# Optimization experiments

Hardware: AMD Instinct MI355X
Metric: run time of the kernel (lower is better)

The kernel has to match this reference:

```python
import jax, jax.numpy as jnp
import numpy as np

# dims derived from init_kwargs
N_NODES = 100000            # type_mask.shape[0]
N0, N1 = 60000, 40000       # nodes per type
F0, F1 = 128, 64            # feats_dim_list
HID = 64                    # hidden_dim (= in_dim of layer1)
HEADS = 8
OUT = 16
ATTN_VEC = 128
E = 250000                  # metapath instances per metapath
L = 3                       # nodes per metapath instance (2 edge types)
NG = 8192                   # nodes in each minibatch DGL graph
B = 8192                    # number of target nodes
ETYPES = [[0, 1], [2, 3]]   # etypes_list; num_edge_type=4, RotatE0 -> 2 base relations


def setup_inputs() -> dict:
    ks = jax.random.split(jax.random.key(0), 20)
    g = lambda k, s, sc=1.0: sc * jax.random.normal(k, s, dtype=jnp.float32)
    return {
        "feat0": g(ks[0], (N0, F0)),
        "feat1": g(ks[1], (N1, F1)),
        "W0": g(ks[2], (HID, F0), 0.12),
        "b0": jnp.zeros((HID,), jnp.float32),
        "W1": g(ks[3], (HID, F1), 0.15),
        "b1": jnp.zeros((HID,), jnp.float32),
        "r_vec": g(ks[4], (2, HID // 2, 2), 0.2),
        "attn0": g(ks[5], (HEADS, HID), 0.2),
        "attn1": g(ks[6], (HEADS, HID), 0.2),
        "fc1_w": g(ks[7], (ATTN_VEC, HEADS * HID), 0.06),
        "fc1_b": jnp.zeros((ATTN_VEC,), jnp.float32),
        "fc2_w": g(ks[8], (1, ATTN_VEC), 0.1),
        "fc_w": g(ks[9], (OUT, HEADS * HID), 0.06),
        "fc_b": jnp.zeros((OUT,), jnp.float32),
        "idx0": jnp.arange(N0, dtype=jnp.int32),                 # type-0 node ids (contiguous block)
        "idx1": jnp.arange(N1, dtype=jnp.int32) + N0,            # type-1 node ids (offset block)
        "mp0_indices": jax.random.randint(ks[10], (E, L), 0, N_NODES, dtype=jnp.int32),
        "mp0_dst": jax.random.randint(ks[11], (E,), 0, NG, dtype=jnp.int32),
        "mp0_target": jax.random.randint(ks[12], (B,), 0, NG, dtype=jnp.int32),
        "mp1_indices": jax.random.randint(ks[13], (E, L), 0, N_NODES, dtype=jnp.int32),
        "mp1_dst": jax.random.randint(ks[14], (E,), 0, NG, dtype=jnp.int32),
        "mp1_target": jax.random.randint(ks[15], (B,), 0, NG, dtype=jnp.int32),
    }


def _cmul(a, b):
    # complex multiply on trailing dim of size 2
    re = a[..., 0] * b[..., 0] - a[..., 1] * b[..., 1]
    im = a[..., 0] * b[..., 1] + a[..., 1] * b[..., 0]
    return jnp.stack([re, im], axis=-1)


def reference(feat0, feat1, W0, b0, W1, b1, r_vec, attn0, attn1,
              fc1_w, fc1_b, fc2_w, fc_w, fc_b,
              idx0, idx1,
              mp0_indices, mp0_dst, mp0_target,
              mp1_indices, mp1_dst, mp1_target):
    # per-node-type linear scattered into a dense [N, HID] table (dropout=0 / eval)
    tf = jnp.zeros((N_NODES, HID), jnp.float32)
    tf = tf.at[idx0].set(feat0 @ W0.T + b0)
    tf = tf.at[idx1].set(feat1 @ W1.T + b1)

    # RotatE0: unit-modulus normalize, then double relations with conjugates
    rv = r_vec / jnp.linalg.norm(r_vec, axis=-1, keepdims=True)          # [2, HID//2, 2]
    conj = rv * jnp.array([1.0, -1.0], rv.dtype)
    rv_full = jnp.stack([rv, conj], axis=1).reshape(-1, HID // 2, 2)     # [4, HID//2, 2]

    def metapath(indices, dst, target, attn, etypes):
        edata = tf[indices].reshape(E, L, HID // 2, 2)   # gather metapath instances
        # suffix products of rotations: final[i] = prod_{j>=i} r[etypes[j]], final[L-1]=1
        final = [jnp.stack([jnp.ones(HID // 2, jnp.float32),
                            jnp.zeros(HID // 2, jnp.float32)], -1)]
        for i in range(L - 2, -1, -1):
            final.insert(0, _cmul(final[0], rv_full[etypes[i]]))
        finals = jnp.stack(final, axis=0)                # [L, HID//2, 2]
        edata = _cmul(edata, finals)                     # rotate every path position
        h = edata.reshape(E, L, HID).mean(axis=1)        # [E, HID] instance encoding
        # node-level attention (heads share h: torch tiles hidden across heads)
        a = jax.nn.leaky_relu(h @ attn.T, 0.01)          # [E, HEADS]
        m = jax.ops.segment_max(a, dst, num_segments=NG)
        ex = jnp.exp(a - m[dst])
        s = jax.ops.segment_sum(ex, dst, num_segments=NG)
        an = ex / s[dst]                                 # edge softmax per destination
        eft = jnp.einsum('eh,ed->ehd', an, h)            # [E, HEADS, HID]
        ft = jax.ops.segment_sum(eft, dst, num_segments=NG)
        ret = ft[target].reshape(B, HEADS * HID)
        return jax.nn.elu(ret)

    out0 = metapath(mp0_indices, mp0_dst, mp0_target, attn0, ETYPES[0])
    out1 = metapath(mp1_indices, mp1_dst, mp1_target, attn1, ETYPES[1])

    # metapath-level attention
    outs = jnp.stack([out0, out1], axis=0)               # [P, B, HEADS*HID]
    s1 = jnp.tanh(outs @ fc1_w.T + fc1_b)                # [P, B, ATTN_VEC]
    beta = jax.nn.softmax((s1.mean(axis=1) @ fc2_w.T)[:, 0], axis=0)  # [P]
    hagg = jnp.einsum('p,pbf->bf', beta, outs)           # [B, HEADS*HID]
    logits = hagg @ fc_w.T + fc_b                        # [B, OUT]
    return logits, hagg
```

## Files before the change

kernel.cpp:

```cpp
#include <hip/hip_runtime.h>
#include <hip/hip_fp16.h>
#include <math.h>

#define NNODES 100000
#define NT0 60000
#define NT1 40000
#define FD0 128
#define FD1 64
#define HID 64
#define HEADS 8
#define OUTD 16
#define AVEC 128
#define NE 250000
#define NG 8192
#define NB 8192

typedef _Float16 half8v __attribute__((ext_vector_type(8)));
typedef float f32x4 __attribute__((ext_vector_type(4)));

#define OFF_TF16    0ull
#define OFF_FINALS  3200000ull
#define OFF_ACC     3200512ull
#define OFF_BETA    3200768ull
#define OFF_WC0     3201024ull
#define OFF_WC1     3208192ull
#define OFF_BC0     3211776ull
#define OFF_BC1     3211904ull
#define OFF_FC1H    3212032ull
#define OFF_P       3244800ull
#define OFF_SORTED  5644800ull
#define OFF_COUNTS  7644800ull
#define OFF_CNTT    7661184ull
#define OFF_CURS    7677568ull
#define OFF_OFFS    7693952ull
#define OFF_FT16    7710592ull

__device__ __forceinline__ float2 rot_pair(const float* r_vec, int pi, int j){
  const float2* rv = (const float2*)r_vec;
  int rel = pi >= 3 ? 1 : 0;
  float2 r = rv[rel*32 + j];
  float n = rsqrtf(r.x*r.x + r.y*r.y);
  r.x *= n; r.y *= n;
  float2 rf = make_float2(r.x, -r.y);
  int pos = pi - rel*3;
  if (pos == 2) return make_float2(1.f, 0.f);
  if (pos == 1) return rf;
  return make_float2(rf.x*r.x - rf.y*r.y, rf.x*r.y + rf.y*r.x);
}

__global__ __launch_bounds__(128) void k_wcat(const float* __restrict__ r_vec,
     const float* __restrict__ attn0, const float* __restrict__ attn1,
     const float* __restrict__ W0v, const float* __restrict__ b0v,
     const float* __restrict__ W1v, const float* __restrict__ b1v,
     const float* __restrict__ fc1_w,
     __half* __restrict__ wc0, float* __restrict__ bc0,
     __half* __restrict__ wc1, float* __restrict__ bc1,
     __half* __restrict__ fc1h,
     float* __restrict__ finals, float* __restrict__ acc, float* __restrict__ beta){
  int bid = blockIdx.x;
  int t = threadIdx.x;
  if (bid == 288){
    if (t < 32){
      float2* F = (float2*)finals;
      #pragma unroll
      for (int pi = 0; pi < 6; ++pi) F[pi*32 + t] = rot_pair(r_vec, pi, t);
    }
    for (int q = t; q < 256; q += 128) acc[q] = 0.f;
    if (t < 2) beta[t] = 0.f;
    return;
  }
  if (bid >= 224){
    int base = (bid - 224)*1024;
    for (int i = t; i < 1024; i += 128)
      fc1h[base + i] = __float2half(fc1_w[base + i]);
    return;
  }
  int type = bid >= 112;
  int c = bid - type*112;
  int F = type ? FD1 : FD0;
  const float* W  = type ? W1v : W0v;
  const float* bv = type ? b1v : b0v;
  __half* wc = type ? wc1 : wc0;
  float* bc  = type ? bc1 : bc0;

  if (c < 64){
    for (int f = t; f < F; f += 128) wc[(size_t)c*F + f] = __float2half(W[(size_t)c*F + f]);
    if (t == 0) bc[c] = bv[c];
    return;
  }
  __shared__ float a[64];
  int cg = c - 64;
  int pi = cg >> 3, k = cg & 7;
  if (t < 32){
    float2 f = rot_pair(r_vec, pi, t);
    const float* at = (pi >= 3) ? attn1 : attn0;
    float a0 = at[k*64 + 2*t], a1 = at[k*64 + 2*t + 1];
    a[2*t]     = (f.x*a0 + f.y*a1) * (1.f/3.f);
    a[2*t + 1] = (f.x*a1 - f.y*a0) * (1.f/3.f);
  }
  __syncthreads();
  for (int f = t; f < F; f += 128){
    float s = 0.f;
    #pragma unroll 16
    for (int d = 0; d < 64; ++d) s += a[d] * W[(size_t)d*F + f];
    wc[(size_t)c*F + f] = __float2half(s);
  }
  if (t == 0){
    float s = 0.f;
    #pragma unroll 16
    for (int d = 0; d < 64; ++d) s += a[d] * bv[d];
    bc[c] = s;
  }
}

__global__ __launch_bounds__(256) void k_tform(const float* __restrict__ feat0,
      const int* __restrict__ idx0, const float* __restrict__ feat1,
      const int* __restrict__ idx1,
      const __half* __restrict__ wc0, const float* __restrict__ bc0,
      const __half* __restrict__ wc1, const float* __restrict__ bc1,
      __half* __restrict__ tf16, __half* __restrict__ P){
  const int nb0 = (NT0 + 63)/64;
  int bid = blockIdx.x;
  const float* feat; const int* idx; const __half* wc; const float* bc;
  int n_nodes, F, m0;
  if (bid < nb0){ feat=feat0; idx=idx0; wc=wc0; bc=bc0; n_nodes=NT0; F=FD0; m0=bid*64; }
  else { feat=feat1; idx=idx1; wc=wc1; bc=bc1; n_nodes=NT1; F=FD1; m0=(bid-nb0)*64; }
  __shared__ int idxs[64];
  __shared__ __half outs[64][120];
  int t = threadIdx.x;
  if (t < 64){
    int gm = m0 + t; if (gm > n_nodes - 1) gm = n_nodes - 1;
    idxs[t] = idx[gm];
  }
  __syncthreads();
  int w = t >> 6, l = t & 63;
  int lr = l & 15, lk = l >> 4;
  int gr = m0 + w*16 + lr; if (gr > n_nodes - 1) gr = n_nodes - 1;
  const float* arow = feat + (size_t)gr*F;

  f32x4 acc7[7];
  #pragma unroll
  for (int ct = 0; ct < 7; ++ct) acc7[ct] = (f32x4){0.f,0.f,0.f,0.f};

  int nk = F >> 5;
  for (int kk = 0; kk < nk; ++kk){
    int koff = kk*32 + lk*8;
    float4 ua = *(const float4*)(arow + koff);
    float4 ub = *(const float4*)(arow + koff + 4);
    half8v a = {(_Float16)ua.x,(_Float16)ua.y,(_Float16)ua.z,(_Float16)ua.w,
                (_Float16)ub.x,(_Float16)ub.y,(_Float16)ub.z,(_Float16)ub.w};
    #pragma unroll
    for (int ct = 0; ct < 7; ++ct){
      half8v b = *(const half8v*)(wc + (size_t)(ct*16 + lr)*F + koff);
      acc7[ct] = __builtin_amdgcn_mfma_f32_16x16x32_f16(a, b, acc7[ct], 0, 0, 0);
    }
  }

  #pragma unroll
  for (int ct = 0; ct < 7; ++ct){
    int col = ct*16 + lr;
    float bvv = bc[col];
    #pragma unroll
    for (int r = 0; r < 4; ++r){
      int nl = w*16 + lk*4 + r;
      outs[nl][col] = __float2half(acc7[ct][r] + bvv);
    }
  }
  __syncthreads();
  #pragma unroll
  for (int u = t; u < 512; u += 256){
    int n = u >> 3, c = u & 7;
    if (m0 + n < n_nodes){
      uint4 v = *(uint4*)&outs[n][c*8];
      *(uint4*)&tf16[(size_t)idxs[n]*64 + c*8] = v;
    }
  }
  for (int u = t; u < 384; u += 256){
    int pp = u >= 192;
    int rr = u - pp*192;
    int n = rr / 3, c = rr - n*3;
    if (m0 + n < n_nodes){
      uint4 v = *(uint4*)&outs[n][64 + pp*24 + c*8];
      *(uint4*)&P[(size_t)pp*2400000 + (size_t)idxs[n]*24 + c*8] = v;
    }
  }
}

__global__ void k_hist3(const int* __restrict__ d0, const int* __restrict__ d1,
                        const int* __restrict__ t0, const int* __restrict__ t1,
                        int* __restrict__ counts, int* __restrict__ cntt){
  int e = blockIdx.x*blockDim.x + threadIdx.x;
  if (e < NE) atomicAdd(&counts[d0[e]], 1);
  else if (e < 2*NE) atomicAdd(&counts[NG + d1[e-NE]], 1);
  else if (e < 2*NE + NB) atomicAdd(&cntt[t0[e-2*NE]], 1);
  else if (e < 2*NE + 2*NB) atomicAdd(&cntt[NG + t1[e-2*NE-NB]], 1);
}

__global__ __launch_bounds__(1024) void k_scan(const int* __restrict__ counts,
                                               int* __restrict__ offs,
                                               int* __restrict__ curs){
  __shared__ int lds[1024];
  int t = threadIdx.x;
  int base = t*16;
  int v[16]; int sum = 0;
  #pragma unroll
  for (int i = 0; i < 16; ++i){ v[i] = counts[base+i]; sum += v[i]; }
  lds[t] = sum;
  __syncthreads();
  for (int off = 1; off < 1024; off <<= 1){
    int x = (t >= off) ? lds[t-off] : 0;
    __syncthreads();
    lds[t] += x;
    __syncthreads();
  }
  int excl = lds[t] - sum;
  #pragma unroll
  for (int i = 0; i < 16; ++i){ offs[base+i] = excl; excl += v[i]; curs[base+i] = 0; }
  if (t == 1023) offs[2*NG] = excl;
}

__global__ void k_scatter2(const int* __restrict__ m0, const int* __restrict__ d0,
                           const int* __restrict__ m1, const int* __restrict__ d1,
                           const int* __restrict__ offs, int* __restrict__ curs,
                           int4* __restrict__ sorted){
  int e = blockIdx.x*blockDim.x + threadIdx.x;
  if (e >= 2*NE) return;
  const int* mp; int d;
  if (e < NE){ mp = m0 + (size_t)e*3; d = d0[e]; }
  else { mp = m1 + (size_t)(e-NE)*3; d = NG + d1[e-NE]; }
  int pos = offs[d] + atomicAdd(&curs[d], 1);
  sorted[pos] = make_int4(mp[0], mp[1], mp[2], 0);
}

__global__ __launch_bounds__(128) void k_seg(const __half* __restrict__ tf16,
                                             const __half* __restrict__ P,
                                             const int4* __restrict__ sorted,
                                             const int* __restrict__ offs,
                                             const float* __restrict__ finals,
                                             __half* __restrict__ ft16o){
  __shared__ int4 ndb[2][64];
  __shared__ float wb[2][64][8];
  int wv = threadIdx.x >> 6;
  int seg = blockIdx.x*2 + wv;
  int p = seg >> 13;
  int lane = threadIdx.x & 63;
  int hw = lane >> 5, j = lane & 31;
  int start = offs[seg], end = offs[seg+1];
  __half2* ftw = (__half2*)(ft16o + (size_t)seg*512);
  if (start == end){
    #pragma unroll
    for (int kk = 0; kk < 4; ++kk) ftw[(hw*4+kk)*32 + j] = __floats2half2_rn(0.f, 0.f);
    return;
  }
  const float2* F2 = (const float2*)(finals + p*192);
  float2 f0 = F2[j], f1 = F2[32 + j];
  const __half2* tfh = (const __half2*)tf16;
  const __half* Pp = P + (size_t)p*2400000;
  int4* nb = ndb[wv];
  float (*wbp)[8] = wb[wv];

  float sA[8], ur[8], ui[8];
  #pragma unroll
  for (int k = 0; k < 8; ++k){ sA[k] = 0.f; ur[k] = 0.f; ui[k] = 0.f; }

  for (int c = start; c < end; c += 64){
    int n = end - c; if (n > 64) n = 64;
    if (lane < n){
      int4 nd = sorted[c + lane];
      nb[lane] = nd;
      float4 rA = *(const float4*)(Pp + (size_t)nd.x*24);
      float4 rB = *(const float4*)(Pp + (size_t)nd.y*24 + 8);
      float4 rC = *(const float4*)(Pp + (size_t)nd.z*24 + 16);
      const __half2* ha = (const __half2*)&rA;
      const __half2* hb = (const __half2*)&rB;
      const __half2* hc = (const __half2*)&rC;
      float w[8];
      #pragma unroll
      for (int m = 0; m < 4; ++m){
        float2 va = __half22float2(ha[m]);
        float2 vb = __half22float2(hb[m]);
        float2 vc = __half22float2(hc[m]);
        float x0 = va.x + vb.x + vc.x;
        float x1 = va.y + vb.y + vc.y;
        x0 = x0 > 0.f ? x0 : 0.01f*x0;
        x1 = x1 > 0.f ? x1 : 0.01f*x1;
        w[2*m]   = __expf(x0);
        w[2*m+1] = __expf(x1);
      }
      #pragma unroll
      for (int k = 0; k < 8; ++k) sA[k] += w[k];
      *(float4*)&wbp[lane][0] = make_float4(w[0], w[1], w[2], w[3]);
      *(float4*)&wbp[lane][4] = make_float4(w[4], w[5], w[6], w[7]);
    }
    asm volatile("s_waitcnt lgkmcnt(0)" ::: "memory");
    __builtin_amdgcn_sched_barrier(0);
    int cend = c + n;
    for (int i = c + hw; i < cend; i += 2){
      int e = i - c;
      int4 nd = nb[e];
      float4 wlo = *(const float4*)&wbp[e][0];
      float4 whi = *(const float4*)&wbp[e][4];
      float2 v0 = __half22float2(tfh[(size_t)nd.x*32 + j]);
      float2 v1 = __half22float2(tfh[(size_t)nd.y*32 + j]);
      float2 v2 = __half22float2(tfh[(size_t)nd.z*32 + j]);
      float hre = (v0.x*f0.x - v0.y*f0.y) + (v1.x*f1.x - v1.y*f1.y) + v2.x;
      float him = (v0.x*f0.y + v0.y*f0.x) + (v1.x*f1.y + v1.y*f1.x) + v2.y;
      ur[0] += wlo.x*hre; ui[0] += wlo.x*him;
      ur[1] += wlo.y*hre; ui[1] += wlo.y*him;
      ur[2] += wlo.z*hre; ui[2] += wlo.z*him;
      ur[3] += wlo.w*hre; ui[3] += wlo.w*him;
      ur[4] += whi.x*hre; ui[4] += whi.x*him;
      ur[5] += whi.y*hre; ui[5] += whi.y*him;
      ur[6] += whi.z*hre; ui[6] += whi.z*him;
      ur[7] += whi.w*hre; ui[7] += whi.w*him;
    }
    asm volatile("s_waitcnt lgkmcnt(0)" ::: "memory");
    __builtin_amdgcn_sched_barrier(0);
  }
  #pragma unroll
  for (int k = 0; k < 8; ++k){
    ur[k] += __shfl_xor(ur[k], 32);
    ui[k] += __shfl_xor(ui[k], 32);
    float v = sA[k];
    #pragma unroll
    for (int mask = 1; mask < 64; mask <<= 1) v += __shfl_xor(v, mask);
    sA[k] = v;
  }
  #pragma unroll
  for (int kk = 0; kk < 4; ++kk){
    int k = hw*4 + kk;
    float inv = 1.f / (3.f * sA[k]);
    float re = ur[k]*inv, im = ui[k]*inv;
    re = re > 0.f ? re : expm1f(re);
    im = im > 0.f ? im : expm1f(im);
    ftw[k*32 + j] = __floats2half2_rn(re, im);
  }
}

__global__ __launch_bounds__(256) void k_s1g(const __half* __restrict__ ft16o,
                                             const int* __restrict__ cntt,
                                             const __half* __restrict__ fc1h,
                                             const float* __restrict__ fc1_b,
                                             float* __restrict__ acc_p){
  int bid = blockIdx.x;
  int p  = bid >> 8;
  int rb = bid & 255;
  int t = threadIdx.x;
  int w = t >> 6, l = t & 63;
  int rowbase = rb*32 + (w & 1)*16;
  int colbase = (w >> 1)*64;
  int lr = l & 15, lk = l >> 4;

  const half8v* Ab = (const half8v*)(ft16o + ((size_t)p*NG + rowbase)*512);
  f32x4 acc[4] = {{0.f,0.f,0.f,0.f},{0.f,0.f,0.f,0.f},
                  {0.f,0.f,0.f,0.f},{0.f,0.f,0.f,0.f}};

  #pragma unroll 4
  for (int kk = 0; kk < 16; ++kk){
    half8v a = Ab[(size_t)lr*64 + kk*4 + lk];
    #pragma unroll
    for (int ct = 0; ct < 4; ++ct){
      const half8v* Bb = (const half8v*)(fc1h + (size_t)(colbase + ct*16 + lr)*512);
      half8v b = Bb[kk*4 + lk];
      acc[ct] = __builtin_amdgcn_mfma_f32_16x16x32_f16(a, b, acc[ct], 0, 0, 0);
    }
  }

  float cf[4];
  #pragma unroll
  for (int r = 0; r < 4; ++r)
    cf[r] = (float)cntt[p*NG + rowbase + lk*4 + r];
  #pragma unroll
  for (int ct = 0; ct < 4; ++ct){
    int col = colbase + ct*16 + lr;
    float bv = fc1_b[col];
    float sv = 0.f;
    #pragma unroll
    for (int r = 0; r < 4; ++r)
      sv += cf[r] * tanhf(acc[ct][r] + bv);
    sv += __shfl_xor(sv, 16);
    sv += __shfl_xor(sv, 32);
    if (l < 16) atomicAdd(&acc_p[p*128 + col], sv);
  }
}

__global__ void k_beta(const float* __restrict__ acc, const float* __restrict__ fc2_w,
                       float* __restrict__ beta){
  int t = threadIdx.x;
  float s0 = acc[t]*fc2_w[t] + acc[t+64]*fc2_w[t+64];
  float s1 = acc[128+t]*fc2_w[t] + acc[192+t]*fc2_w[t+64];
  #pragma unroll
  for (int mask = 1; mask < 64; mask <<= 1){
    s0 += __shfl_xor(s0, mask, 64);
    s1 += __shfl_xor(s1, mask, 64);
  }
  if (t == 0){
    float z0 = s0 / (float)NB, z1 = s1 / (float)NB;
    float mz = fmaxf(z0, z1);
    float e0 = expf(z0 - mz), e1 = expf(z1 - mz);
    float inv = 1.f / (e0 + e1);
    beta[0] = e0*inv; beta[1] = e1*inv;
  }
}

__global__ void k_final(const __half* __restrict__ ft0, const __half* __restrict__ ft1,
                        const int* __restrict__ tgt0, const int* __restrict__ tgt1,
                        const float* __restrict__ beta, const float* __restrict__ fc_w,
                        const float* __restrict__ fc_b, float* __restrict__ d_out){
  __shared__ float lds[512];
  int b = blockIdx.x, t = threadIdx.x;
  float b0 = beta[0], b1 = beta[1];
  int g0 = tgt0[b], g1 = tgt1[b];
  float v0 = __half2float(ft0[(size_t)g0*512 + t]);
  float v1 = __half2float(ft1[(size_t)g1*512 + t]);
  float h = b0*v0 + b1*v1;
  lds[t] = h;
  d_out[(size_t)NB*OUTD + (size_t)b*512 + t] = h;
  __syncthreads();
  int o = t >> 5, j = t & 31;
  float s = 0.f;
  const float* w = fc_w + o*512;
  for (int d = j; d < 512; d += 32) s += lds[d]*w[d];
  #pragma unroll
  for (int mask = 1; mask < 32; mask <<= 1) s += __shfl_xor(s, mask, 32);
  if (j == 0) d_out[(size_t)b*OUTD + o] = s + fc_b[o];
}

extern "C" void kernel_launch(void* const* d_in, const int* in_sizes, int n_in,
                              void* d_out, int out_size, void* d_ws, size_t ws_size,
                              hipStream_t stream){
  const float* feat0  = (const float*)d_in[0];
  const float* feat1  = (const float*)d_in[1];
  const float* W0     = (const float*)d_in[2];
  const float* b0     = (const float*)d_in[3];
  const float* W1     = (const float*)d_in[4];
  const float* b1     = (const float*)d_in[5];
  const float* r_vec  = (const float*)d_in[6];
  const float* attn0  = (const float*)d_in[7];
  const float* attn1  = (const float*)d_in[8];
  const float* fc1_w  = (const float*)d_in[9];
  const float* fc1_b  = (const float*)d_in[10];
  const float* fc2_w  = (const float*)d_in[11];
  const float* fc_w   = (const float*)d_in[12];
  const float* fc_b   = (const float*)d_in[13];
  const int*   idx0   = (const int*)d_in[14];
  const int*   idx1   = (const int*)d_in[15];
  const int*   mpi0   = (const int*)d_in[16];
  const int*   mdst0  = (const int*)d_in[17];
  const int*   mtgt0  = (const int*)d_in[18];
  const int*   mpi1   = (const int*)d_in[19];
  const int*   mdst1  = (const int*)d_in[20];
  const int*   mtgt1  = (const int*)d_in[21];

  float* ws      = (float*)d_ws;
  __half* tf16   = (__half*)(ws + OFF_TF16);
  float* finals  = ws + OFF_FINALS;
  float* acc     = ws + OFF_ACC;
  float* beta    = ws + OFF_BETA;
  __half* wc0    = (__half*)(ws + OFF_WC0);
  __half* wc1    = (__half*)(ws + OFF_WC1);
  float* bc0     = ws + OFF_BC0;
  float* bc1     = ws + OFF_BC1;
  __half* fc1h   = (__half*)(ws + OFF_FC1H);
  __half* P      = (__half*)(ws + OFF_P);
  int4*  sorted  = (int4*)(ws + OFF_SORTED);
  int*   counts  = (int*)(ws + OFF_COUNTS);
  int*   cntt    = (int*)(ws + OFF_CNTT);
  int*   curs    = (int*)(ws + OFF_CURS);
  int*   offs    = (int*)(ws + OFF_OFFS);
  __half* ft16o  = (__half*)(ws + OFF_FT16);
  __half* ft0h   = ft16o;
  __half* ft1h   = ft16o + (size_t)NG*512;

  k_wcat<<<289, 128, 0, stream>>>(r_vec, attn0, attn1, W0, b0, W1, b1, fc1_w,
                                  wc0, bc0, wc1, bc1, fc1h, finals, acc, beta);
  hipMemsetAsync(counts, 0, 2*16384*sizeof(int), stream);
  k_hist3<<<(2*NE + 2*NB + 255)/256, 256, 0, stream>>>(mdst0, mdst1, mtgt0, mtgt1,
                                                       counts, cntt);
  k_scan<<<1, 1024, 0, stream>>>(counts, offs, curs);
  k_scatter2<<<(2*NE + 255)/256, 256, 0, stream>>>(mpi0, mdst0, mpi1, mdst1,
                                                   offs, curs, sorted);

  k_tform<<<(NT0 + 63)/64 + (NT1 + 63)/64, 256, 0, stream>>>(
      feat0, idx0, feat1, idx1, wc0, bc0, wc1, bc1, tf16, P);

  k_seg<<<NG, 128, 0, stream>>>(tf16, P, sorted, offs, finals, ft16o);

  k_s1g<<<512, 256, 0, stream>>>(ft16o, cntt, fc1h, fc1_b, acc);
  k_beta<<<1, 64, 0, stream>>>(acc, fc2_w, beta);
  k_final<<<NB, 512, 0, stream>>>(ft0h, ft1h, mtgt0, mtgt1, beta, fc_w, fc_b,
                                  (float*)d_out);
}
```

Before: 225.6 us.

## Precompute per-node output projection via MFMA and fold memset into setup kernel

The final fc projection is linear, so it is applied to every segment node's features inside the fc1 MFMA kernel, with an extra MFMA accumulator on half the waves. The final kernel then combines two 16-wide rows per target using beta instead of running a 512-wide dot product through LDS. The counts memset and the fc_w fp16 conversion move into extra blocks of the setup kernel, which removes an API call. An unroll pragma is also added to the segment aggregation loop. The trade-off is fp16 weights for the output projection and more work in k_s1g.

```diff
diff --git a/kernel.cpp b/kernel.cpp
--- a/kernel.cpp
+++ b/kernel.cpp
@@ -34,6 +34,8 @@
 #define OFF_CURS    7677568ull
 #define OFF_OFFS    7693952ull
 #define OFF_FT16    7710592ull
+#define OFF_L       11904896ull
+#define OFF_FCWH    12167040ull
 
 __device__ __forceinline__ float2 rot_pair(const float* r_vec, int pi, int j){
   const float2* rv = (const float2*)r_vec;
@@ -52,13 +54,24 @@
      const float* __restrict__ attn0, const float* __restrict__ attn1,
      const float* __restrict__ W0v, const float* __restrict__ b0v,
      const float* __restrict__ W1v, const float* __restrict__ b1v,
-     const float* __restrict__ fc1_w,
+     const float* __restrict__ fc1_w, const float* __restrict__ fc_w,
      __half* __restrict__ wc0, float* __restrict__ bc0,
      __half* __restrict__ wc1, float* __restrict__ bc1,
-     __half* __restrict__ fc1h,
+     __half* __restrict__ fc1h, __half* __restrict__ fcwh,
+     int* __restrict__ counts,
      float* __restrict__ finals, float* __restrict__ acc, float* __restrict__ beta){
   int bid = blockIdx.x;
   int t = threadIdx.x;
+  if (bid == 297){
+    for (int i = t; i < OUTD*512; i += 128) fcwh[i] = __float2half(fc_w[i]);
+    return;
+  }
+  if (bid >= 289){
+    int base = (bid - 289)*4096;
+    #pragma unroll
+    for (int i = t; i < 4096; i += 128) counts[base + i] = 0;
+    return;
+  }
   if (bid == 288){
     if (t < 32){
       float2* F = (float2*)finals;
@@ -295,6 +308,7 @@
     asm volatile("s_waitcnt lgkmcnt(0)" ::: "memory");
     __builtin_amdgcn_sched_barrier(0);
     int cend = c + n;
+    #pragma unroll 2
     for (int i = c + hw; i < cend; i += 2){
       int e = i - c;
       int4 nd = nb[e];
@@ -341,6 +355,8 @@
                                              const int* __restrict__ cntt,
                                              const __half* __restrict__ fc1h,
                                              const float* __restrict__ fc1_b,
+                                             const __half* __restrict__ fcwh,
+                                             float* __restrict__ Lb,
                                              float* __restrict__ acc_p){
   int bid = blockIdx.x;
   int p  = bid >> 8;
@@ -350,10 +366,12 @@
   int rowbase = rb*32 + (w & 1)*16;
   int colbase = (w >> 1)*64;
   int lr = l & 15, lk = l >> 4;
+  bool doL = (w >> 1) == 0;
 
   const half8v* Ab = (const half8v*)(ft16o + ((size_t)p*NG + rowbase)*512);
   f32x4 acc[4] = {{0.f,0.f,0.f,0.f},{0.f,0.f,0.f,0.f},
                   {0.f,0.f,0.f,0.f},{0.f,0.f,0.f,0.f}};
+  f32x4 accL = {0.f,0.f,0.f,0.f};
 
   #pragma unroll 4
   for (int kk = 0; kk < 16; ++kk){
@@ -363,6 +381,10 @@
       const half8v* Bb = (const half8v*)(fc1h + (size_t)(colbase + ct*16 + lr)*512);
       half8v b = Bb[kk*4 + lk];
       acc[ct] = __builtin_amdgcn_mfma_f32_16x16x32_f16(a, b, acc[ct], 0, 0, 0);
+    }
+    if (doL){
+      half8v b = *(const half8v*)(fcwh + (size_t)lr*512 + kk*32 + lk*8);
+      accL = __builtin_amdgcn_mfma_f32_16x16x32_f16(a, b, accL, 0, 0, 0);
     }
   }
 
@@ -381,6 +403,11 @@
     sv += __shfl_xor(sv, 16);
     sv += __shfl_xor(sv, 32);
     if (l < 16) atomicAdd(&acc_p[p*128 + col], sv);
+  }
+  if (doL){
+    #pragma unroll
+    for (int r = 0; r < 4; ++r)
+      Lb[((size_t)p*NG + rowbase + lk*4 + r)*16 + lr] = accL[r];
   }
 }
 
@@ -405,25 +432,18 @@
 
 __global__ void k_final(const __half* __restrict__ ft0, const __half* __restrict__ ft1,
                         const int* __restrict__ tgt0, const int* __restrict__ tgt1,
-                        const float* __restrict__ beta, const float* __restrict__ fc_w,
+                        const float* __restrict__ beta, const float* __restrict__ Lb,
                         const float* __restrict__ fc_b, float* __restrict__ d_out){
-  __shared__ float lds[512];
   int b = blockIdx.x, t = threadIdx.x;
   float b0 = beta[0], b1 = beta[1];
   int g0 = tgt0[b], g1 = tgt1[b];
   float v0 = __half2float(ft0[(size_t)g0*512 + t]);
   float v1 = __half2float(ft1[(size_t)g1*512 + t]);
-  float h = b0*v0 + b1*v1;
-  lds[t] = h;
-  d_out[(size_t)NB*OUTD + (size_t)b*512 + t] = h;
-  __syncthreads();
-  int o = t >> 5, j = t & 31;
-  float s = 0.f;
-  const float* w = fc_w + o*512;
-  for (int d = j; d < 512; d += 32) s += lds[d]*w[d];
-  #pragma unroll
-  for (int mask = 1; mask < 32; mask <<= 1) s += __shfl_xor(s, mask, 32);
-  if (j == 0) d_out[(size_t)b*OUTD + o] = s + fc_b[o];
+  d_out[(size_t)NB*OUTD + (size_t)b*512 + t] = b0*v0 + b1*v1;
+  if (t < OUTD){
+    float lv = b0*Lb[(size_t)g0*16 + t] + b1*Lb[((size_t)NG + g1)*16 + t] + fc_b[t];
+    d_out[(size_t)b*OUTD + t] = lv;
+  }
 }
 
 extern "C" void kernel_launch(void* const* d_in, const int* in_sizes, int n_in,
@@ -471,10 +491,12 @@
   __half* ft16o  = (__half*)(ws + OFF_FT16);
   __half* ft0h   = ft16o;
   __half* ft1h   = ft16o + (size_t)NG*512;
-
-  k_wcat<<<289, 128, 0, stream>>>(r_vec, attn0, attn1, W0, b0, W1, b1, fc1_w,
-                                  wc0, bc0, wc1, bc1, fc1h, finals, acc, beta);
-  hipMemsetAsync(counts, 0, 2*16384*sizeof(int), stream);
+  float* Lb      = ws + OFF_L;
+  __half* fcwh   = (__half*)(ws + OFF_FCWH);
+
+  k_wcat<<<298, 128, 0, stream>>>(r_vec, attn0, attn1, W0, b0, W1, b1, fc1_w, fc_w,
+                                  wc0, bc0, wc1, bc1, fc1h, fcwh, counts,
+                                  finals, acc, beta);
   k_hist3<<<(2*NE + 2*NB + 255)/256, 256, 0, stream>>>(mdst0, mdst1, mtgt0, mtgt1,
                                                        counts, cntt);
   k_scan<<<1, 1024, 0, stream>>>(counts, offs, curs);
@@ -486,8 +508,8 @@
 
   k_seg<<<NG, 128, 0, stream>>>(tf16, P, sorted, offs, finals, ft16o);
 
-  k_s1g<<<512, 256, 0, stream>>>(ft16o, cntt, fc1h, fc1_b, acc);
+  k_s1g<<<512, 256, 0, stream>>>(ft16o, cntt, fc1h, fc1_b, fcwh, Lb, acc);
   k_beta<<<1, 64, 0, stream>>>(acc, fc2_w, beta);
-  k_final<<<NB, 512, 0, stream>>>(ft0h, ft1h, mtgt0, mtgt1, beta, fc_w, fc_b,
+  k_final<<<NB, 512, 0, stream>>>(ft0h, ft1h, mtgt0, mtgt1, beta, Lb, fc_b,
                                   (float*)d_out);
 }
```

New measurement: 215.2 us. 1.05x faster.
